# Kernel optimization log

Hardware: AMD Instinct MI355X
Metric: run time of the kernel (lower is better)

The kernel has to match this reference:

```python
import jax, jax.numpy as jnp
import numpy as np

DIM = 768
HEADS = 12
HEAD_DIM = DIM // HEADS
SCALE = HEAD_DIM ** -0.5


def setup_inputs() -> dict:
    key = jax.random.key(0)
    ks = jax.random.split(key, 5)
    x = jax.random.normal(ks[0], (2, 4096, DIM), dtype=jnp.float32)
    # torch nn.Linear params: weight [out, in], bias [out]
    qkv_w = jax.random.normal(ks[1], (3 * DIM, DIM), dtype=jnp.float32) * (DIM ** -0.5)
    qkv_b = jax.random.normal(ks[2], (3 * DIM,), dtype=jnp.float32) * 0.02
    proj_w = jax.random.normal(ks[3], (DIM, DIM), dtype=jnp.float32) * (DIM ** -0.5)
    proj_b = jax.random.normal(ks[4], (DIM,), dtype=jnp.float32) * 0.02
    return {"x": x, "qkv_w": qkv_w, "qkv_b": qkv_b, "proj_w": proj_w, "proj_b": proj_b}


def reference(x, qkv_w, qkv_b, proj_w, proj_b):
    b, n, c = x.shape
    qkv = x @ qkv_w.T + qkv_b                      # [b, n, 3c]
    qkv = qkv.reshape(b, n, 3, HEADS, HEAD_DIM)
    qkv = jnp.transpose(qkv, (2, 0, 3, 1, 4))      # [3, b, h, n, d]
    q, k, v = qkv[0], qkv[1], qkv[2]
    attn = jax.nn.softmax(jnp.einsum('bhqd,bhkd->bhqk', q, k) * SCALE, axis=-1)
    out = jnp.einsum('bhqk,bhkd->bhqd', attn, v)   # [b, h, n, d]
    out = jnp.transpose(out, (0, 2, 1, 3)).reshape(b, n, c)
    return out @ proj_w.T + proj_b
```

## Files before the change

### kernel.cpp

```cpp
#include <hip/hip_runtime.h>
#include <stdint.h>

#define SEQ   4096
#define NDIM  768
#define HD    64
#define NH    12
#define NBH   24
#define MTOT  8192

#define LSTR 40
#define PSTR 72

typedef short s8v __attribute__((ext_vector_type(8)));
typedef float f4v __attribute__((ext_vector_type(4)));
typedef unsigned short u16;
typedef u16 u16x4 __attribute__((ext_vector_type(4)));

typedef uint32_t u32x2a __attribute__((ext_vector_type(2), may_alias));
typedef short    s8va   __attribute__((ext_vector_type(8), may_alias));

#define C1 0.18033688011112042f

__device__ __forceinline__ u16 f2bf(float f) {
  union { float f; uint32_t u; } cv; cv.f = f;
  const uint32_t u = cv.u;
  return (u16)((u + 0x7fffu + ((u >> 16) & 1u)) >> 16);
}
__device__ __forceinline__ float ex2(float x) { return __builtin_amdgcn_exp2f(x); }
__device__ __forceinline__ uint32_t fbits(float f) {
  union { float f; uint32_t u; } cv; cv.f = f; return cv.u;
}

__global__ __launch_bounds__(256) void cvt3_kernel(
    const float* __restrict__ a, u16* __restrict__ da, int na4,
    const float* __restrict__ b, u16* __restrict__ db, int nb4,
    const float* __restrict__ c, u16* __restrict__ dc, int nc4) {
  int i = blockIdx.x * 256 + threadIdx.x;
  const float* s; u16* d;
  if (i < na4)             { s = a; d = da; }
  else if (i < na4 + nb4)  { s = b; d = db; i -= na4; }
  else if (i < na4 + nb4 + nc4) { s = c; d = dc; i -= na4 + nb4; }
  else return;
  const float4 f = ((const float4*)s)[i];
  u16x4 r;
  r[0] = f2bf(f.x); r[1] = f2bf(f.y); r[2] = f2bf(f.z); r[3] = f2bf(f.w);
  ((u16x4*)d)[i] = r;
}

__global__ __launch_bounds__(256) void gemm_qkv(const u16* __restrict__ A,
    const u16* __restrict__ B, const float* __restrict__ bias,
    u16* __restrict__ qg, u16* __restrict__ kg, u16* __restrict__ vtg) {
  __shared__ __align__(16) u16 at[128 * LSTR];
  __shared__ __align__(16) u16 bt[128 * LSTR];
  const int tid  = threadIdx.x;
  const int lane = tid & 63;
  const int w    = tid >> 6;
  const int quad = lane >> 4;
  const int col  = lane & 15;
  const int m0 = blockIdx.y * 128;
  const int n0 = blockIdx.x * 128;
  const int srow = tid >> 2;
  const int sch  = (tid & 3) * 8;
  const int wm = (w >> 1) * 64;
  const int wn = (w & 1) * 64;

  const f4v fz = {0.f, 0.f, 0.f, 0.f};
  f4v acc[4][4];
#pragma unroll
  for (int i = 0; i < 4; i++)
#pragma unroll
    for (int j = 0; j < 4; j++) acc[i][j] = fz;

  const u16* ap0 = A + (size_t)(m0 + srow) * NDIM + sch;
  const u16* ap1 = A + (size_t)(m0 + 64 + srow) * NDIM + sch;
  const u16* bp0 = B + (size_t)(n0 + srow) * NDIM + sch;
  const u16* bp1 = B + (size_t)(n0 + 64 + srow) * NDIM + sch;

  for (int k0 = 0; k0 < NDIM; k0 += 32) {
    const s8v va0 = *(const s8v*)(ap0 + k0);
    const s8v va1 = *(const s8v*)(ap1 + k0);
    const s8v vb0 = *(const s8v*)(bp0 + k0);
    const s8v vb1 = *(const s8v*)(bp1 + k0);
    __syncthreads();
    *(s8v*)(at + srow * LSTR + sch) = va0;
    *(s8v*)(at + (64 + srow) * LSTR + sch) = va1;
    *(s8v*)(bt + srow * LSTR + sch) = vb0;
    *(s8v*)(bt + (64 + srow) * LSTR + sch) = vb1;
    __syncthreads();
    s8v af[4], bf[4];
#pragma unroll
    for (int i = 0; i < 4; i++)
      af[i] = *(const s8v*)(at + (wm + i * 16 + col) * LSTR + quad * 8);
#pragma unroll
    for (int j = 0; j < 4; j++)
      bf[j] = *(const s8v*)(bt + (wn + j * 16 + col) * LSTR + quad * 8);
#pragma unroll
    for (int i = 0; i < 4; i++)
#pragma unroll
      for (int j = 0; j < 4; j++)
        acc[i][j] = __builtin_amdgcn_mfma_f32_16x16x32_bf16(af[i], bf[j], acc[i][j], 0, 0, 0);
  }

  const int wmg = m0 + wm;
  const int wng = n0 + wn;
  const int s = n0 / NDIM;
#pragma unroll
  for (int j = 0; j < 4; j++) {
    const int c = wng + j * 16 + col;
    const float bv = bias[c];
    const int r = c - s * NDIM;
    const int h = r >> 6;
    const int d = r & 63;
#pragma unroll
    for (int i = 0; i < 4; i++) {
      const int mb = wmg + i * 16 + quad * 4;
      const int bb = mb >> 12;
      const int n  = mb & 4095;
      const size_t hb = (size_t)(bb * NH + h);
      const f4v v = acc[i][j];
      if (s == 2) {
        u16x4 pk;
#pragma unroll
        for (int rg = 0; rg < 4; rg++) pk[rg] = f2bf(v[rg] + bv);
        *(u16x4*)(vtg + (hb * HD + d) * SEQ + n) = pk;
      } else if (s == 0) {
#pragma unroll
        for (int rg = 0; rg < 4; rg++)
          qg[(hb * SEQ + (size_t)(n + rg)) * HD + d] = f2bf((v[rg] + bv) * C1);
      } else {
#pragma unroll
        for (int rg = 0; rg < 4; rg++)
          kg[(hb * SEQ + (size_t)(n + rg)) * HD + d] = f2bf(v[rg] + bv);
      }
    }
  }
}

__global__ __launch_bounds__(256) void attn_kernel(const u16* __restrict__ qg,
    const u16* __restrict__ kg, const u16* __restrict__ vtg, u16* __restrict__ og) {
  __shared__ __align__(16) u16 kls[64 * PSTR];
  __shared__ __align__(16) u16 vls[64 * PSTR];
  __shared__ __align__(16) u16 pls[128 * PSTR];

  const int tid  = threadIdx.x;
  const int lane = tid & 63;
  const int w    = tid >> 6;
  const int quad = lane >> 4;
  const int col  = lane & 15;
  const int blk = blockIdx.x;
  const int bh  = blk % NBH;
  const int q0  = (blk / NBH) * 128;
  const size_t gbase = (size_t)bh * (SEQ * HD);
  const int wq = w * 32;

  s8v qf[2][2];
#pragma unroll
  for (int s = 0; s < 2; s++)
#pragma unroll
    for (int qt = 0; qt < 2; qt++)
      qf[s][qt] = *(const s8v*)(qg + gbase +
          (size_t)(q0 + wq + qt * 16 + col) * HD + s * 32 + quad * 8);

  const f4v fz = {0.f, 0.f, 0.f, 0.f};
  f4v l4[2] = {fz, fz};
  f4v o[4][2];
#pragma unroll
  for (int dt = 0; dt < 4; dt++)
#pragma unroll
    for (int qt = 0; qt < 2; qt++) o[dt][qt] = fz;

  const int srow8 = tid >> 3;
  const int sch8  = (tid & 7) * 8;
  const u16* kp = kg  + gbase + (size_t)srow8 * HD  + sch8;
  const u16* vp = vtg + gbase + (size_t)srow8 * SEQ;
  u16* const prow = pls + (wq + col) * PSTR;

  s8v kr0 = *(const s8v*)(kp);
  s8v kr1 = *(const s8v*)(kp + (size_t)32 * HD);
  s8v vr0 = *(const s8v*)(vp + sch8);
  s8v vr1 = *(const s8v*)(vp + (size_t)32 * SEQ + sch8);

  for (int kb = 0; kb < SEQ; kb += 64) {
    __syncthreads();
    *(s8v*)(kls + srow8 * PSTR + sch8) = kr0;
    *(s8v*)(kls + (32 + srow8) * PSTR + sch8) = kr1;
    *(s8v*)(vls + srow8 * PSTR + sch8) = vr0;
    *(s8v*)(vls + (32 + srow8) * PSTR + sch8) = vr1;
    __syncthreads();

    if (kb + 64 < SEQ) {
      kr0 = *(const s8v*)(kp + (size_t)(kb + 64) * HD);
      kr1 = *(const s8v*)(kp + (size_t)(kb + 96) * HD);
      vr0 = *(const s8v*)(vp + kb + 64 + sch8);
      vr1 = *(const s8v*)(vp + (size_t)32 * SEQ + kb + 64 + sch8);
    }

    f4v st[4][2];
#pragma unroll
    for (int kt = 0; kt < 4; kt++)
#pragma unroll
      for (int qt = 0; qt < 2; qt++) st[kt][qt] = fz;
#pragma unroll
    for (int s = 0; s < 2; s++) {
#pragma unroll
      for (int kt = 0; kt < 4; kt++) {
        const s8v ak = *(const s8v*)(kls + (kt * 16 + col) * PSTR + s * 32 + quad * 8);
#pragma unroll
        for (int qt = 0; qt < 2; qt++)
          st[kt][qt] = __builtin_amdgcn_mfma_f32_16x16x32_bf16(ak, qf[s][qt], st[kt][qt], 0, 0, 0);
      }
    }

#pragma unroll
    for (int qt = 0; qt < 2; qt++) {
      u16* const pq = prow + qt * 16 * PSTR;
#pragma unroll
      for (int kt = 0; kt < 4; kt++) {
        f4v p;
#pragma unroll
        for (int rg = 0; rg < 4; rg++) p[rg] = ex2(st[kt][qt][rg]);
        l4[qt] += p;
        const uint32_t u0 = fbits(p[0]) + 0x8000u;
        const uint32_t u1 = fbits(p[1]) + 0x8000u;
        const uint32_t u2 = fbits(p[2]) + 0x8000u;
        const uint32_t u3 = fbits(p[3]) + 0x8000u;
        u32x2a wv;
        wv.x = __builtin_amdgcn_perm(u1, u0, 0x07060302u);
        wv.y = __builtin_amdgcn_perm(u3, u2, 0x07060302u);
        *(u32x2a*)(pq + kt * 16 + quad * 4) = wv;
      }
    }
    asm volatile("" ::: "memory");

#pragma unroll
    for (int s = 0; s < 2; s++) {
      s8va bp[2];
#pragma unroll
      for (int qt = 0; qt < 2; qt++)
        bp[qt] = *(const s8va*)(prow + qt * 16 * PSTR + s * 32 + quad * 8);
#pragma unroll
      for (int dt = 0; dt < 4; dt++) {
        const s8v av = *(const s8v*)(vls + (dt * 16 + col) * PSTR + s * 32 + quad * 8);
#pragma unroll
        for (int qt = 0; qt < 2; qt++)
          o[dt][qt] = __builtin_amdgcn_mfma_f32_16x16x32_bf16(av, (s8v)bp[qt], o[dt][qt], 0, 0, 0);
      }
    }
    asm volatile("" ::: "memory");
  }

  const int b = bh / NH;
  const int h = bh % NH;
#pragma unroll
  for (int qt = 0; qt < 2; qt++) {
    float l = l4[qt][0] + l4[qt][1] + l4[qt][2] + l4[qt][3];
    l += __shfl_xor(l, 16);
    l += __shfl_xor(l, 32);
    const float inv = 1.0f / l;
    const int qi = q0 + wq + qt * 16 + col;
    u16* rowp = og + (size_t)(b * SEQ + qi) * NDIM + h * HD;
#pragma unroll
    for (int dt = 0; dt < 4; dt++) {
      u16x4 pk;
#pragma unroll
      for (int rg = 0; rg < 4; rg++) pk[rg] = f2bf(o[dt][qt][rg] * inv);
      *(u16x4*)(rowp + dt * 16 + quad * 4) = pk;
    }
  }
}

__global__ __launch_bounds__(256) void gemm_proj(const u16* __restrict__ A,
    const u16* __restrict__ B, const float* __restrict__ bias, float* __restrict__ out) {
  __shared__ __align__(16) u16 at[128 * LSTR];
  __shared__ __align__(16) u16 bt[128 * LSTR];
  const int tid  = threadIdx.x;
  const int lane = tid & 63;
  const int w    = tid >> 6;
  const int quad = lane >> 4;
  const int col  = lane & 15;
  const int m0 = blockIdx.y * 128;
  const int n0 = blockIdx.x * 128;
  const int srow = tid >> 2;
  const int sch  = (tid & 3) * 8;
  const int wm = (w >> 1) * 64;
  const int wn = (w & 1) * 64;

  const f4v fz = {0.f, 0.f, 0.f, 0.f};
  f4v acc[4][4];
#pragma unroll
  for (int i = 0; i < 4; i++)
#pragma unroll
    for (int j = 0; j < 4; j++) acc[i][j] = fz;

  const u16* ap0 = A + (size_t)(m0 + srow) * NDIM + sch;
  const u16* ap1 = A + (size_t)(m0 + 64 + srow) * NDIM + sch;
  const u16* bp0 = B + (size_t)(n0 + srow) * NDIM + sch;
  const u16* bp1 = B + (size_t)(n0 + 64 + srow) * NDIM + sch;

  for (int k0 = 0; k0 < NDIM; k0 += 32) {
    const s8v va0 = *(const s8v*)(ap0 + k0);
    const s8v va1 = *(const s8v*)(ap1 + k0);
    const s8v vb0 = *(const s8v*)(bp0 + k0);
    const s8v vb1 = *(const s8v*)(bp1 + k0);
    __syncthreads();
    *(s8v*)(at + srow * LSTR + sch) = va0;
    *(s8v*)(at + (64 + srow) * LSTR + sch) = va1;
    *(s8v*)(bt + srow * LSTR + sch) = vb0;
    *(s8v*)(bt + (64 + srow) * LSTR + sch) = vb1;
    __syncthreads();
    s8v af[4], bf[4];
#pragma unroll
    for (int i = 0; i < 4; i++)
      af[i] = *(const s8v*)(at + (wm + i * 16 + col) * LSTR + quad * 8);
#pragma unroll
    for (int j = 0; j < 4; j++)
      bf[j] = *(const s8v*)(bt + (wn + j * 16 + col) * LSTR + quad * 8);
#pragma unroll
    for (int i = 0; i < 4; i++)
#pragma unroll
      for (int j = 0; j < 4; j++)
        acc[i][j] = __builtin_amdgcn_mfma_f32_16x16x32_bf16(af[i], bf[j], acc[i][j], 0, 0, 0);
  }

  const int wmg = m0 + wm;
  const int wng = n0 + wn;
#pragma unroll
  for (int j = 0; j < 4; j++) {
    const int c = wng + j * 16 + col;
    const float bv = bias[c];
#pragma unroll
    for (int i = 0; i < 4; i++) {
#pragma unroll
      for (int rg = 0; rg < 4; rg++)
        out[(size_t)(wmg + i * 16 + quad * 4 + rg) * NDIM + c] = acc[i][j][rg] + bv;
    }
  }
}

extern "C" void kernel_launch(void* const* d_in, const int* in_sizes, int n_in,
                              void* d_out, int out_size, void* d_ws, size_t ws_size,
                              hipStream_t stream) {
  const float* x      = (const float*)d_in[0];
  const float* qkv_w  = (const float*)d_in[1];
  const float* qkv_b  = (const float*)d_in[2];
  const float* proj_w = (const float*)d_in[3];
  const float* proj_b = (const float*)d_in[4];
  float* out = (float*)d_out;

  u16* ws   = (u16*)d_ws;
  u16* x_bf = ws;
  u16* wq   = x_bf + (size_t)MTOT * NDIM;
  u16* wp   = wq + (size_t)3 * NDIM * NDIM;
  u16* q_bf = wp + (size_t)NDIM * NDIM;
  u16* k_bf = q_bf + (size_t)NBH * SEQ * HD;
  u16* vt   = k_bf + (size_t)NBH * SEQ * HD;
  u16* a_bf = vt + (size_t)NBH * SEQ * HD;

  const int nx = MTOT * NDIM / 4, nw1 = 3 * NDIM * NDIM / 4, nw2 = NDIM * NDIM / 4;
  const int ntot = nx + nw1 + nw2;
  cvt3_kernel<<<(ntot + 255) / 256, 256, 0, stream>>>(x, x_bf, nx, qkv_w, wq, nw1,
                                                      proj_w, wp, nw2);

  gemm_qkv<<<dim3(18, 64), 256, 0, stream>>>(x_bf, wq, qkv_b, q_bf, k_bf, vt);
  attn_kernel<<<768, 256, 0, stream>>>(q_bf, k_bf, vt, a_bf);
  gemm_proj<<<dim3(6, 64), 256, 0, stream>>>(a_bf, wp, proj_b, out);
}
```

Before: 303.8 us.

## Switch attention to 32x32x16 MFMA with register-resident P and double-buffered K/V

```diff
diff --git a/kernel.cpp b/kernel.cpp
--- a/kernel.cpp
+++ b/kernel.cpp
@@ -13,11 +13,11 @@
 
 typedef short s8v __attribute__((ext_vector_type(8)));
 typedef float f4v __attribute__((ext_vector_type(4)));
+typedef float f16x __attribute__((ext_vector_type(16)));
 typedef unsigned short u16;
 typedef u16 u16x4 __attribute__((ext_vector_type(4)));
-
-typedef uint32_t u32x2a __attribute__((ext_vector_type(2), may_alias));
-typedef short    s8va   __attribute__((ext_vector_type(8), may_alias));
+typedef uint32_t u32x4v __attribute__((ext_vector_type(4)));
+typedef int i32x2 __attribute__((ext_vector_type(2)));
 
 #define C1 0.18033688011112042f
 
@@ -27,8 +27,15 @@
   return (u16)((u + 0x7fffu + ((u >> 16) & 1u)) >> 16);
 }
 __device__ __forceinline__ float ex2(float x) { return __builtin_amdgcn_exp2f(x); }
-__device__ __forceinline__ uint32_t fbits(float f) {
-  union { float f; uint32_t u; } cv; cv.f = f; return cv.u;
+
+__device__ __forceinline__ uint32_t cvtpk_bf16(float lo, float hi) {
+  uint32_t r;
+  asm("v_cvt_pk_bf16_f32 %0, %1, %2" : "=v"(r) : "v"(lo), "v"(hi));
+  return r;
+}
+__device__ __forceinline__ void pl32swap(uint32_t& a, uint32_t& b) {
+  i32x2 r = __builtin_amdgcn_permlane32_swap((int)a, (int)b, false, false);
+  a = (uint32_t)r.x; b = (uint32_t)r.y;
 }
 
 __global__ __launch_bounds__(256) void cvt3_kernel(
@@ -136,56 +143,51 @@
   }
 }
 
-__global__ __launch_bounds__(256) void attn_kernel(const u16* __restrict__ qg,
+__global__ __launch_bounds__(256, 3) void attn_kernel(const u16* __restrict__ qg,
     const u16* __restrict__ kg, const u16* __restrict__ vtg, u16* __restrict__ og) {
-  __shared__ __align__(16) u16 kls[64 * PSTR];
-  __shared__ __align__(16) u16 vls[64 * PSTR];
-  __shared__ __align__(16) u16 pls[128 * PSTR];
+  __shared__ __align__(16) u16 kls[2][64 * PSTR];
+  __shared__ __align__(16) u16 vls[2][64 * PSTR];
+  __shared__ float lws[4][32];
 
   const int tid  = threadIdx.x;
   const int lane = tid & 63;
   const int w    = tid >> 6;
-  const int quad = lane >> 4;
-  const int col  = lane & 15;
+  const int hi   = lane >> 5;
+  const int c    = lane & 31;
   const int blk = blockIdx.x;
   const int bh  = blk % NBH;
   const int q0  = (blk / NBH) * 128;
   const size_t gbase = (size_t)bh * (SEQ * HD);
   const int wq = w * 32;
 
-  s8v qf[2][2];
-#pragma unroll
-  for (int s = 0; s < 2; s++)
-#pragma unroll
-    for (int qt = 0; qt < 2; qt++)
-      qf[s][qt] = *(const s8v*)(qg + gbase +
-          (size_t)(q0 + wq + qt * 16 + col) * HD + s * 32 + quad * 8);
-
-  const f4v fz = {0.f, 0.f, 0.f, 0.f};
-  f4v l4[2] = {fz, fz};
-  f4v o[4][2];
-#pragma unroll
-  for (int dt = 0; dt < 4; dt++)
-#pragma unroll
-    for (int qt = 0; qt < 2; qt++) o[dt][qt] = fz;
+  s8v qf[4];
+#pragma unroll
+  for (int s = 0; s < 4; s++)
+    qf[s] = *(const s8v*)(qg + gbase + (size_t)(q0 + wq + c) * HD + s * 16 + hi * 8);
+
+  f16x o0, o1;
+#pragma unroll
+  for (int e = 0; e < 16; e++) { o0[e] = 0.f; o1[e] = 0.f; }
+  float l0 = 0.f, l1 = 0.f, l2 = 0.f, l3 = 0.f;
 
   const int srow8 = tid >> 3;
   const int sch8  = (tid & 7) * 8;
   const u16* kp = kg  + gbase + (size_t)srow8 * HD  + sch8;
   const u16* vp = vtg + gbase + (size_t)srow8 * SEQ;
-  u16* const prow = pls + (wq + col) * PSTR;
 
   s8v kr0 = *(const s8v*)(kp);
   s8v kr1 = *(const s8v*)(kp + (size_t)32 * HD);
   s8v vr0 = *(const s8v*)(vp + sch8);
   s8v vr1 = *(const s8v*)(vp + (size_t)32 * SEQ + sch8);
+  *(s8v*)(kls[0] + srow8 * PSTR + sch8) = kr0;
+  *(s8v*)(kls[0] + (32 + srow8) * PSTR + sch8) = kr1;
+  *(s8v*)(vls[0] + srow8 * PSTR + sch8) = vr0;
+  *(s8v*)(vls[0] + (32 + srow8) * PSTR + sch8) = vr1;
 
   for (int kb = 0; kb < SEQ; kb += 64) {
-    __syncthreads();
-    *(s8v*)(kls + srow8 * PSTR + sch8) = kr0;
-    *(s8v*)(kls + (32 + srow8) * PSTR + sch8) = kr1;
-    *(s8v*)(vls + srow8 * PSTR + sch8) = vr0;
-    *(s8v*)(vls + (32 + srow8) * PSTR + sch8) = vr1;
+    const int cur = (kb >> 6) & 1;
+    const u16* kt_ = kls[cur];
+    const u16* vt_ = vls[cur];
     __syncthreads();
 
     if (kb + 64 < SEQ) {
@@ -195,77 +197,99 @@
       vr1 = *(const s8v*)(vp + (size_t)32 * SEQ + kb + 64 + sch8);
     }
 
-    f4v st[4][2];
-#pragma unroll
-    for (int kt = 0; kt < 4; kt++)
-#pragma unroll
-      for (int qt = 0; qt < 2; qt++) st[kt][qt] = fz;
-#pragma unroll
-    for (int s = 0; s < 2; s++) {
-#pragma unroll
-      for (int kt = 0; kt < 4; kt++) {
-        const s8v ak = *(const s8v*)(kls + (kt * 16 + col) * PSTR + s * 32 + quad * 8);
-#pragma unroll
-        for (int qt = 0; qt < 2; qt++)
-          st[kt][qt] = __builtin_amdgcn_mfma_f32_16x16x32_bf16(ak, qf[s][qt], st[kt][qt], 0, 0, 0);
-      }
-    }
-
-#pragma unroll
-    for (int qt = 0; qt < 2; qt++) {
-      u16* const pq = prow + qt * 16 * PSTR;
-#pragma unroll
-      for (int kt = 0; kt < 4; kt++) {
-        f4v p;
-#pragma unroll
-        for (int rg = 0; rg < 4; rg++) p[rg] = ex2(st[kt][qt][rg]);
-        l4[qt] += p;
-        const uint32_t u0 = fbits(p[0]) + 0x8000u;
-        const uint32_t u1 = fbits(p[1]) + 0x8000u;
-        const uint32_t u2 = fbits(p[2]) + 0x8000u;
-        const uint32_t u3 = fbits(p[3]) + 0x8000u;
-        u32x2a wv;
-        wv.x = __builtin_amdgcn_perm(u1, u0, 0x07060302u);
-        wv.y = __builtin_amdgcn_perm(u3, u2, 0x07060302u);
-        *(u32x2a*)(pq + kt * 16 + quad * 4) = wv;
-      }
-    }
-    asm volatile("" ::: "memory");
-
-#pragma unroll
-    for (int s = 0; s < 2; s++) {
-      s8va bp[2];
-#pragma unroll
-      for (int qt = 0; qt < 2; qt++)
-        bp[qt] = *(const s8va*)(prow + qt * 16 * PSTR + s * 32 + quad * 8);
-#pragma unroll
-      for (int dt = 0; dt < 4; dt++) {
-        const s8v av = *(const s8v*)(vls + (dt * 16 + col) * PSTR + s * 32 + quad * 8);
-#pragma unroll
-        for (int qt = 0; qt < 2; qt++)
-          o[dt][qt] = __builtin_amdgcn_mfma_f32_16x16x32_bf16(av, (s8v)bp[qt], o[dt][qt], 0, 0, 0);
-      }
-    }
-    asm volatile("" ::: "memory");
-  }
+    f16x st0, st1;
+#pragma unroll
+    for (int e = 0; e < 16; e++) { st0[e] = 0.f; st1[e] = 0.f; }
+#pragma unroll
+    for (int s = 0; s < 4; s++) {
+      const s8v k0 = *(const s8v*)(kt_ + c * PSTR + s * 16 + hi * 8);
+      const s8v k1 = *(const s8v*)(kt_ + (32 + c) * PSTR + s * 16 + hi * 8);
+      st0 = __builtin_amdgcn_mfma_f32_32x32x16_bf16(k0, qf[s], st0, 0, 0, 0);
+      st1 = __builtin_amdgcn_mfma_f32_32x32x16_bf16(k1, qf[s], st1, 0, 0, 0);
+    }
+
+    s8v pa0, pa1, pa2, pa3;
+    {
+      float p[16];
+#pragma unroll
+      for (int e = 0; e < 16; e++) p[e] = ex2(st0[e]);
+      l0 += p[0] + p[4] + p[8]  + p[12];
+      l1 += p[1] + p[5] + p[9]  + p[13];
+      l2 += p[2] + p[6] + p[10] + p[14];
+      l3 += p[3] + p[7] + p[11] + p[15];
+      uint32_t k0 = cvtpk_bf16(p[0],  p[1]);
+      uint32_t k1 = cvtpk_bf16(p[2],  p[3]);
+      uint32_t k2 = cvtpk_bf16(p[4],  p[5]);
+      uint32_t k3 = cvtpk_bf16(p[6],  p[7]);
+      uint32_t k4 = cvtpk_bf16(p[8],  p[9]);
+      uint32_t k5 = cvtpk_bf16(p[10], p[11]);
+      uint32_t k6 = cvtpk_bf16(p[12], p[13]);
+      uint32_t k7 = cvtpk_bf16(p[14], p[15]);
+      pl32swap(k0, k2); pl32swap(k1, k3);
+      pl32swap(k4, k6); pl32swap(k5, k7);
+      u32x4v wA = {k0, k1, k2, k3};
+      u32x4v wB = {k4, k5, k6, k7};
+      pa0 = __builtin_bit_cast(s8v, wA);
+      pa1 = __builtin_bit_cast(s8v, wB);
+    }
+    {
+      float p[16];
+#pragma unroll
+      for (int e = 0; e < 16; e++) p[e] = ex2(st1[e]);
+      l0 += p[0] + p[4] + p[8]  + p[12];
+      l1 += p[1] + p[5] + p[9]  + p[13];
+      l2 += p[2] + p[6] + p[10] + p[14];
+      l3 += p[3] + p[7] + p[11] + p[15];
+      uint32_t k0 = cvtpk_bf16(p[0],  p[1]);
+      uint32_t k1 = cvtpk_bf16(p[2],  p[3]);
+      uint32_t k2 = cvtpk_bf16(p[4],  p[5]);
+      uint32_t k3 = cvtpk_bf16(p[6],  p[7]);
+      uint32_t k4 = cvtpk_bf16(p[8],  p[9]);
+      uint32_t k5 = cvtpk_bf16(p[10], p[11]);
+      uint32_t k6 = cvtpk_bf16(p[12], p[13]);
+      uint32_t k7 = cvtpk_bf16(p[14], p[15]);
+      pl32swap(k0, k2); pl32swap(k1, k3);
+      pl32swap(k4, k6); pl32swap(k5, k7);
+      u32x4v wA = {k0, k1, k2, k3};
+      u32x4v wB = {k4, k5, k6, k7};
+      pa2 = __builtin_bit_cast(s8v, wA);
+      pa3 = __builtin_bit_cast(s8v, wB);
+    }
+
+#pragma unroll
+    for (int ks = 0; ks < 4; ks++) {
+      const s8v pv = ks == 0 ? pa0 : ks == 1 ? pa1 : ks == 2 ? pa2 : pa3;
+      const s8v v0 = *(const s8v*)(vt_ + c * PSTR + ks * 16 + hi * 8);
+      const s8v v1 = *(const s8v*)(vt_ + (32 + c) * PSTR + ks * 16 + hi * 8);
+      o0 = __builtin_amdgcn_mfma_f32_32x32x16_bf16(pv, v0, o0, 0, 0, 0);
+      o1 = __builtin_amdgcn_mfma_f32_32x32x16_bf16(pv, v1, o1, 0, 0, 0);
+    }
+
+    if (kb + 64 < SEQ) {
+      u16* kn = (u16*)kls[cur ^ 1];
+      u16* vn = (u16*)vls[cur ^ 1];
+      *(s8v*)(kn + srow8 * PSTR + sch8) = kr0;
+      *(s8v*)(kn + (32 + srow8) * PSTR + sch8) = kr1;
+      *(s8v*)(vn + srow8 * PSTR + sch8) = vr0;
+      *(s8v*)(vn + (32 + srow8) * PSTR + sch8) = vr1;
+    }
+  }
+
+  float lt = l0 + l1 + l2 + l3;
+  lt += __shfl_xor(lt, 32);
+  const float inv = 1.0f / lt;
+  if (hi == 0) lws[w][c] = inv;
 
   const int b = bh / NH;
   const int h = bh % NH;
-#pragma unroll
-  for (int qt = 0; qt < 2; qt++) {
-    float l = l4[qt][0] + l4[qt][1] + l4[qt][2] + l4[qt][3];
-    l += __shfl_xor(l, 16);
-    l += __shfl_xor(l, 32);
-    const float inv = 1.0f / l;
-    const int qi = q0 + wq + qt * 16 + col;
-    u16* rowp = og + (size_t)(b * SEQ + qi) * NDIM + h * HD;
-#pragma unroll
-    for (int dt = 0; dt < 4; dt++) {
-      u16x4 pk;
-#pragma unroll
-      for (int rg = 0; rg < 4; rg++) pk[rg] = f2bf(o[dt][qt][rg] * inv);
-      *(u16x4*)(rowp + dt * 16 + quad * 4) = pk;
-    }
+  u16* obase = og + (size_t)(b * SEQ + q0 + wq) * NDIM + h * HD + c;
+#pragma unroll
+  for (int r = 0; r < 16; r++) {
+    const int row = (r & 3) + 8 * (r >> 2) + 4 * hi;
+    const float invr = lws[w][row];
+    u16* rp = obase + (size_t)row * NDIM;
+    rp[0]  = f2bf(o0[r] * invr);
+    rp[32] = f2bf(o1[r] * invr);
   }
 }
 
```

Result: faster. 285.2 us (-6.1%).
